# Kernel tuning notes

Hardware: AMD Instinct MI355X
Metric: run time of the kernel (lower is better)

The kernel has to match this reference:

```python
import jax, jax.numpy as jnp
import numpy as np

# ---- static config (matches init_kwargs) ----
N, E = 8192, 262144
IN_CH, MP_CH, HID, K = 128, 512, 256, 10
EPS, DELTA = 1e-3, 0.311
TV_COEFF, BAL_COEFF = 0.785, 0.514


def setup_inputs() -> dict:
    key = jax.random.key(0)
    ks = jax.random.split(key, 16)

    def p(k, shape):
        fan_in = shape[0] if len(shape) > 1 else shape[0]
        return (jax.random.normal(k, shape, jnp.float32) / np.sqrt(fan_in)).astype(jnp.float32)

    return {
        "x": jax.random.normal(ks[0], (N, IN_CH), jnp.float32),
        "edge_index": jax.random.randint(ks[1], (2, E), 0, N, jnp.int32),
        "edge_weight": jax.random.uniform(ks[2], (E,), jnp.float32),
        # GTVConv layer 1 / 2 (Linear weight + bias)
        "W1": p(ks[3], (IN_CH, MP_CH)), "b1": jnp.zeros((MP_CH,), jnp.float32),
        "W2": p(ks[4], (MP_CH, MP_CH)), "b2": jnp.zeros((MP_CH,), jnp.float32),
        # pooling MLP [512 -> 256 -> K], relu, no norm
        "Wm1": p(ks[5], (MP_CH, HID)), "bm1": jnp.zeros((HID,), jnp.float32),
        "Wm2": p(ks[6], (HID, K)), "bm2": jnp.zeros((K,), jnp.float32),
    }


def _gtv_conv(x, src, dst, w, W, b):
    """GTVConv: out = elu( h - delta*(D_G h - Gamma h) + b ),
    gamma_ij = w_ij / max(||h_i - h_j||_1, eps), h = x @ W."""
    h = x @ W                                   # [N, C]
    diff = jnp.sum(jnp.abs(h[src] - h[dst]), axis=-1)   # [E]
    gamma = w / jnp.maximum(diff, EPS)                  # [E]
    deg = jnp.zeros(h.shape[0], h.dtype).at[dst].add(gamma)          # [N]
    agg = jnp.zeros_like(h).at[dst].add(gamma[:, None] * h[src])     # Gamma @ h
    out = h - DELTA * (deg[:, None] * h - agg) + b
    return jax.nn.elu(out)


def reference(x, edge_index, edge_weight, W1, b1, W2, b2, Wm1, bm1, Wm2, bm2):
    src, dst = edge_index[0], edge_index[1]

    h = _gtv_conv(x, src, dst, edge_weight, W1, b1)
    h = _gtv_conv(h, src, dst, edge_weight, W2, b2)

    # pooling MLP -> cluster logits s
    s_logits = jax.nn.relu(h @ Wm1 + bm1) @ Wm2 + bm2   # [N, K]

    # dense adjacency (to_dense_adj: duplicate edges accumulate)
    adj = jnp.zeros((N, N), x.dtype).at[src, dst].add(edge_weight)

    s = jax.nn.softmax(s_logits, axis=-1)

    # total-variation loss: sum_ij a_ij * sum_k |s_ik - s_jk| / (2 * nnz(adj))
    tv = jnp.zeros((), x.dtype)
    for k in range(K):  # small fixed loop over clusters, avoids [N,N,K] tensor
        col = s[:, k]
        tv = tv + jnp.sum(adj * jnp.abs(col[:, None] - col[None, :]))
    n_edges = jax.lax.stop_gradient(jnp.count_nonzero(adj).astype(x.dtype))
    tv = tv / (2.0 * n_edges)

    # asymmetric-norm balance loss (AsymCheegerCut)
    idx = N // K + 1                         # rho-quantile index (static)
    quant = jnp.sort(s, axis=0)[N - idx]     # idx-th largest per cluster, [K]
    t = s - quant[None, :]
    asym = jnp.where(t >= 0, (K - 1) * t, -t)
    denom = float(N * (K - 1))
    bal = (denom - jnp.sum(asym)) / denom

    return s_logits, TV_COEFF * tv, BAL_COEFF * bal
```

## Files before the change

kernel.cpp:

```cpp
#include <hip/hip_runtime.h>

#define N_NODES 8192
#define N_EDGES 262144
#define IN_CH 128
#define MP_CH 512
#define HID 256
#define KCL 10
#define EPS_C 0.001f
#define DELTA_C 0.311f
#define TV_COEFF_C 0.785f
#define BAL_COEFF_C 0.514f
#define RANK1 7373

typedef __bf16 bf16x8 __attribute__((ext_vector_type(8)));
typedef float f32x4 __attribute__((ext_vector_type(4)));
typedef unsigned short ushort8 __attribute__((ext_vector_type(8)));

__device__ __forceinline__ float bf2f(unsigned short h) {
  union { unsigned int u; float f; } c; c.u = ((unsigned int)h) << 16; return c.f;
}
__device__ __forceinline__ unsigned short f2bf(float f) {
  union { float f; unsigned int u; } c; c.f = f;
  unsigned int r = c.u + 0x7fffu + ((c.u >> 16) & 1u);
  return (unsigned short)(r >> 16);
}

__global__ void prep_kernel(const float* __restrict__ x, const float* __restrict__ W1,
                            const float* __restrict__ W2, const float* __restrict__ Wm1,
                            unsigned short* __restrict__ xb, unsigned short* __restrict__ W1bt,
                            unsigned short* __restrict__ W2bt, unsigned short* __restrict__ Wm1bt,
                            const int* __restrict__ dst, int* __restrict__ cnt) {
  int i = blockIdx.x * 256 + threadIdx.x;
  if (i < 1048576) { xb[i] = f2bf(x[i]); return; }
  i -= 1048576;
  if (i < 65536) { int n = i >> 7, k = i & 127; W1bt[i] = f2bf(W1[k * MP_CH + n]); return; }
  i -= 65536;
  if (i < 262144) { int n = i >> 9, k = i & 511; W2bt[i] = f2bf(W2[k * MP_CH + n]); return; }
  i -= 262144;
  if (i < 131072) { int n = i >> 9, k = i & 511; Wm1bt[i] = f2bf(Wm1[k * HID + n]); return; }
  i -= 131072;
  if (i < N_EDGES) atomicAdd(&cnt[dst[i]], 1);
}

__global__ __launch_bounds__(1024) void scan_kernel(const int* __restrict__ cnt,
                                                    int* __restrict__ offs,
                                                    int* __restrict__ cursor) {
  __shared__ int ts[1024];
  int t = threadIdx.x;
  int v[8]; int s = 0;
#pragma unroll
  for (int j = 0; j < 8; ++j) { v[j] = cnt[t * 8 + j]; s += v[j]; }
  ts[t] = s; __syncthreads();
  for (int off = 1; off < 1024; off <<= 1) {
    int add = (t >= off) ? ts[t - off] : 0;
    __syncthreads();
    ts[t] += add;
    __syncthreads();
  }
  int base = ts[t] - s;
#pragma unroll
  for (int j = 0; j < 8; ++j) { offs[t * 8 + j] = base; cursor[t * 8 + j] = base; base += v[j]; }
  if (t == 1023) offs[N_NODES] = ts[1023];
}

__global__ void fill_kernel(const int* __restrict__ src, const int* __restrict__ dst,
                            const float* __restrict__ ew, int* __restrict__ cursor,
                            int2* __restrict__ esw) {
  for (int e = blockIdx.x * blockDim.x + threadIdx.x; e < N_EDGES; e += gridDim.x * blockDim.x) {
    int p = atomicAdd(&cursor[dst[e]], 1);
    esw[p] = make_int2(src[e], __float_as_int(ew[e]));
  }
}

__global__ __launch_bounds__(256) void gemm_bt(
    const unsigned short* __restrict__ A, const unsigned short* __restrict__ BT,
    float* __restrict__ C, unsigned short* __restrict__ Cb,
    const float* __restrict__ bias, int N, int K, int epi) {
  __shared__ unsigned short lsm[2 * 128 * 32];
  unsigned short* lA = lsm;
  unsigned short* lB = lsm + 128 * 32;
  int lane = threadIdx.x & 63;
  int wv = threadIdx.x >> 6;
  int tm = blockIdx.y * 128, tn = blockIdx.x * 128;
  int wm = (wv >> 1) * 64, wn = (wv & 1) * 64;
  int rA = lane & 15, quad = lane >> 4;
  f32x4 acc[4][4];
#pragma unroll
  for (int i = 0; i < 4; ++i)
#pragma unroll
    for (int j = 0; j < 4; ++j) acc[i][j] = (f32x4){0.f, 0.f, 0.f, 0.f};

  int arow = wv * 32 + (lane >> 2);
  int acol = (lane & 3) * 8;

  for (int k0 = 0; k0 < K; k0 += 32) {
#pragma unroll
    for (int c = 0; c < 2; ++c) {
      const unsigned short* ga = A + (size_t)(tm + arow + c * 16) * K + k0 + acol;
      __builtin_amdgcn_global_load_lds(
          (const __attribute__((address_space(1))) unsigned int*)ga,
          (__attribute__((address_space(3))) unsigned int*)(lA + (wv * 32 + c * 16) * 32),
          16, 0, 0);
      const unsigned short* gb = BT + (size_t)(tn + arow + c * 16) * K + k0 + acol;
      __builtin_amdgcn_global_load_lds(
          (const __attribute__((address_space(1))) unsigned int*)gb,
          (__attribute__((address_space(3))) unsigned int*)(lB + (wv * 32 + c * 16) * 32),
          16, 0, 0);
    }
    __syncthreads();
    bf16x8 af[4], bfr[4];
#pragma unroll
    for (int i = 0; i < 4; ++i)
      af[i] = *(const bf16x8*)(lA + (wm + i * 16 + rA) * 32 + quad * 8);
#pragma unroll
    for (int j = 0; j < 4; ++j)
      bfr[j] = *(const bf16x8*)(lB + (wn + j * 16 + rA) * 32 + quad * 8);
#pragma unroll
    for (int i = 0; i < 4; ++i)
#pragma unroll
      for (int j = 0; j < 4; ++j)
        acc[i][j] = __builtin_amdgcn_mfma_f32_16x16x32_bf16(af[i], bfr[j], acc[i][j], 0, 0, 0);
    __syncthreads();
  }

  if (epi == 1) {
#pragma unroll
    for (int i = 0; i < 4; ++i)
#pragma unroll
      for (int j = 0; j < 4; ++j)
#pragma unroll
        for (int r = 0; r < 4; ++r) {
          int row = tm + wm + i * 16 + quad * 4 + r;
          int col = tn + wn + j * 16 + rA;
          float v = acc[i][j][r] + bias[col];
          C[(size_t)row * N + col] = fmaxf(v, 0.f);
        }
  } else {
    float* fbuf = (float*)lsm;
    int band = threadIdx.x >> 7;
    int rrow = (threadIdx.x >> 3) & 15;
    int cg = threadIdx.x & 7;
#pragma unroll
    for (int i = 0; i < 4; ++i) {
#pragma unroll
      for (int j = 0; j < 4; ++j)
#pragma unroll
        for (int r = 0; r < 4; ++r)
          fbuf[(wv >> 1) * (16 * 128) + (quad * 4 + r) * 128 + (wn + j * 16 + rA)] =
              acc[i][j][r];
      __syncthreads();
      const float* sr = fbuf + band * (16 * 128) + rrow * 128 + cg * 16;
      unsigned short ov[16];
#pragma unroll
      for (int c = 0; c < 16; ++c) ov[c] = f2bf(sr[c]);
      size_t base = (size_t)(tm + band * 64 + i * 16 + rrow) * N + tn + cg * 16;
      *(ushort8*)(Cb + base) = *(ushort8*)ov;
      *(ushort8*)(Cb + base + 8) = *(ushort8*)(ov + 8);
      __syncthreads();
    }
  }
}

__global__ __launch_bounds__(256, 8) void gtv_node(
    const unsigned short* __restrict__ hb, const float* __restrict__ bias,
    const int2* __restrict__ esw, const int* __restrict__ offs,
    unsigned short* __restrict__ outb) {
  int lane = threadIdx.x & 63;
  int wv = threadIdx.x >> 6;
  int d = __builtin_amdgcn_readfirstlane(blockIdx.x * 4 + wv);
  ushort8 hdv = ((const ushort8*)(hb + (size_t)d * MP_CH))[lane];
  float hd[8], acc[8];
#pragma unroll
  for (int j = 0; j < 8; ++j) { hd[j] = bf2f(hdv[j]); acc[j] = 0.f; }
  int e0 = offs[d], e1 = offs[d + 1];
  int i = e0;
  for (; i + 1 < e1; i += 2) {
    int2 ma = esw[i], mb = esw[i + 1];
    float wa = __int_as_float(ma.y), wb = __int_as_float(mb.y);
    ushort8 va = ((const ushort8*)(hb + (size_t)ma.x * MP_CH))[lane];
    ushort8 vb = ((const ushort8*)(hb + (size_t)mb.x * MP_CH))[lane];
    float pa = 0.f, pb = 0.f;
#pragma unroll
    for (int j = 0; j < 8; ++j) {
      pa += fabsf(hd[j] - bf2f(va[j]));
      pb += fabsf(hd[j] - bf2f(vb[j]));
    }
#pragma unroll
    for (int m = 1; m < 64; m <<= 1) { pa += __shfl_xor(pa, m, 64); pb += __shfl_xor(pb, m, 64); }
    float ga = wa * __builtin_amdgcn_rcpf(fmaxf(pa, EPS_C));
    float gb = wb * __builtin_amdgcn_rcpf(fmaxf(pb, EPS_C));
#pragma unroll
    for (int j = 0; j < 8; ++j)
      acc[j] += ga * (hd[j] - bf2f(va[j])) + gb * (hd[j] - bf2f(vb[j]));
  }
  if (i < e1) {
    int2 m0 = esw[i];
    float w = __int_as_float(m0.y);
    ushort8 sv = ((const ushort8*)(hb + (size_t)m0.x * MP_CH))[lane];
    float part = 0.f;
#pragma unroll
    for (int j = 0; j < 8; ++j) part += fabsf(hd[j] - bf2f(sv[j]));
#pragma unroll
    for (int m = 1; m < 64; m <<= 1) part += __shfl_xor(part, m, 64);
    float g = w * __builtin_amdgcn_rcpf(fmaxf(part, EPS_C));
#pragma unroll
    for (int j = 0; j < 8; ++j) acc[j] += g * (hd[j] - bf2f(sv[j]));
  }
  const f32x4* br = (const f32x4*)(bias + lane * 8);
  f32x4 b0 = br[0], b1 = br[1];
  unsigned short ov[8];
#pragma unroll
  for (int j = 0; j < 8; ++j) {
    float bv = (j < 4) ? b0[j] : b1[j - 4];
    float o = hd[j] - DELTA_C * acc[j] + bv;
    o = (o > 0.f) ? o : (expf(o) - 1.f);
    ov[j] = f2bf(o);
  }
  *((ushort8*)(outb + (size_t)d * MP_CH) + lane) = *(ushort8*)ov;
}

__global__ __launch_bounds__(256) void gemm_small(
    const float* __restrict__ hm, const float* __restrict__ W,
    const float* __restrict__ b, float* __restrict__ out, float* __restrict__ s) {
  __shared__ float lw[HID * KCL];
  __shared__ float lb[KCL];
  for (int i = threadIdx.x; i < HID * KCL; i += 256) lw[i] = W[i];
  if (threadIdx.x < KCL) lb[threadIdx.x] = b[threadIdx.x];
  __syncthreads();
  int lane = threadIdx.x & 63, wv = threadIdx.x >> 6;
  int row = blockIdx.x * 4 + wv;
  f32x4 hv = *(const f32x4*)(hm + (size_t)row * HID + lane * 4);
  float p[KCL];
#pragma unroll
  for (int n = 0; n < KCL; ++n) {
    int k0 = lane * 4;
    p[n] = hv[0] * lw[(k0 + 0) * KCL + n] + hv[1] * lw[(k0 + 1) * KCL + n] +
           hv[2] * lw[(k0 + 2) * KCL + n] + hv[3] * lw[(k0 + 3) * KCL + n];
  }
#pragma unroll
  for (int n = 0; n < KCL; ++n)
#pragma unroll
    for (int m = 1; m < 64; m <<= 1) p[n] += __shfl_xor(p[n], m, 64);
  if (lane == 0) {
    float vv[KCL]; float mx = -1e30f;
#pragma unroll
    for (int n = 0; n < KCL; ++n) {
      vv[n] = p[n] + lb[n];
      out[(size_t)row * KCL + n] = vv[n];
      mx = fmaxf(mx, vv[n]);
    }
    float sum = 0.f;
#pragma unroll
    for (int n = 0; n < KCL; ++n) { vv[n] = expf(vv[n] - mx); sum += vv[n]; }
    float inv = 1.f / sum;
#pragma unroll
    for (int n = 0; n < KCL; ++n) s[(size_t)row * KCL + n] = vv[n] * inv;
  }
}

__global__ __launch_bounds__(1024) void tvquant_kernel(
    const int* __restrict__ src, const int* __restrict__ dst,
    const float* __restrict__ ew, const float* __restrict__ s,
    unsigned int* __restrict__ bitmap, float* __restrict__ scal) {
  __shared__ float fsh[16];
  __shared__ int wcnt[2][16];
  int t = threadIdx.x;
  int lane = t & 63, wv = t >> 6;
  if (blockIdx.x < 246) {
    float local = 0.f;
    for (int e = blockIdx.x * 1024 + t; e < N_EDGES; e += 246 * 1024) {
      int a = src[e], b = dst[e];
      float w = ew[e];
      const float* sa = s + (size_t)a * KCL;
      const float* sb = s + (size_t)b * KCL;
      float tv = 0.f;
#pragma unroll
      for (int k = 0; k < KCL; ++k) tv += fabsf(sa[k] - sb[k]);
      local += w * tv;
      if (w != 0.f) {
        unsigned int key = ((unsigned int)a << 13) | (unsigned int)b;
        atomicOr(&bitmap[key >> 5], 1u << (key & 31u));
      }
    }
#pragma unroll
    for (int m = 1; m < 64; m <<= 1) local += __shfl_xor(local, m, 64);
    if (lane == 0) fsh[wv] = local;
    __syncthreads();
    if (t == 0) {
      float tot = 0.f;
#pragma unroll
      for (int i2 = 0; i2 < 16; ++i2) tot += fsh[i2];
      atomicAdd(&scal[0], tot);
    }
  } else {
    int k = blockIdx.x - 246;
    unsigned int v[8];
#pragma unroll
    for (int j = 0; j < 8; ++j)
      v[j] = __float_as_uint(s[(size_t)(t + j * 1024) * KCL + k]);
    unsigned int lo = 0u, hi = 0x3F800000u;
    int p = 0;
    while (lo < hi) {
      unsigned int mid = (lo + hi) >> 1;
      int c = 0;
#pragma unroll
      for (int j = 0; j < 8; ++j) c += (v[j] <= mid) ? 1 : 0;
#pragma unroll
      for (int m = 1; m < 64; m <<= 1) c += __shfl_xor(c, m, 64);
      if (lane == 0) wcnt[p][wv] = c;
      __syncthreads();
      int tot = 0;
#pragma unroll
      for (int i2 = 0; i2 < 16; ++i2) tot += wcnt[p][i2];
      if (tot >= RANK1) hi = mid; else lo = mid + 1;
      p ^= 1;
    }
    float q = __uint_as_float(lo);
    float local = 0.f;
#pragma unroll
    for (int j = 0; j < 8; ++j) {
      float tt = __uint_as_float(v[j]) - q;
      local += (tt >= 0.f) ? 9.f * tt : -tt;
    }
#pragma unroll
    for (int m = 1; m < 64; m <<= 1) local += __shfl_xor(local, m, 64);
    if (lane == 0) fsh[wv] = local;
    __syncthreads();
    if (t == 0) {
      float tot = 0.f;
#pragma unroll
      for (int i2 = 0; i2 < 16; ++i2) tot += fsh[i2];
      atomicAdd(&scal[1], tot);
    }
  }
}

__global__ __launch_bounds__(1024) void popcfin_kernel(const unsigned int* __restrict__ bm,
                                                       float* __restrict__ scal,
                                                       float* __restrict__ out) {
  __shared__ int ish[16];
  int t = threadIdx.x;
  int lane = t & 63, wv = t >> 6;
  int local = 0;
  for (int i = blockIdx.x * 1024 + t; i < (1 << 21); i += 256 * 1024)
    local += __popc(bm[i]);
#pragma unroll
  for (int m = 1; m < 64; m <<= 1) local += __shfl_xor(local, m, 64);
  if (lane == 0) ish[wv] = local;
  __syncthreads();
  if (t == 0) {
    int tot = 0;
#pragma unroll
    for (int i2 = 0; i2 < 16; ++i2) tot += ish[i2];
    atomicAdd((int*)(scal + 2), tot);
    __threadfence();
    int d = atomicAdd((int*)(scal + 3), 1);
    if (d == 255) {
      float tv = scal[0], asym = scal[1];
      float nedges = (float)(*(int*)(scal + 2));
      out[N_NODES * KCL] = TV_COEFF_C * (tv / (2.f * nedges));
      out[N_NODES * KCL + 1] = BAL_COEFF_C * ((73728.f - asym) / 73728.f);
    }
  }
}

#define OFF_BM     ((size_t)0)
#define OFF_CNT    ((size_t)8388608)
#define OFF_SCAL   ((size_t)8421376)
#define OFF_OFFS   ((size_t)8421888)
#define OFF_CURSOR ((size_t)8454912)
#define OFF_HB     ((size_t)16777216)
#define OFF_OUTB   ((size_t)25165824)
#define OFF_HM     ((size_t)33554432)
#define OFF_XB     ((size_t)41943040)
#define OFF_W1BT   ((size_t)44040192)
#define OFF_W2BT   ((size_t)44171264)
#define OFF_WM1BT  ((size_t)44695552)
#define OFF_S      ((size_t)44957696)

extern "C" void kernel_launch(void* const* d_in, const int* in_sizes, int n_in,
                              void* d_out, int out_size, void* d_ws, size_t ws_size,
                              hipStream_t stream) {
  const float* x   = (const float*)d_in[0];
  const int*   ei  = (const int*)d_in[1];
  const float* ew  = (const float*)d_in[2];
  const float* W1  = (const float*)d_in[3];
  const float* b1  = (const float*)d_in[4];
  const float* W2  = (const float*)d_in[5];
  const float* b2  = (const float*)d_in[6];
  const float* Wm1 = (const float*)d_in[7];
  const float* bm1 = (const float*)d_in[8];
  const float* Wm2 = (const float*)d_in[9];
  const float* bm2 = (const float*)d_in[10];
  float* out = (float*)d_out;

  char* ws = (char*)d_ws;
  unsigned int*   bitmap = (unsigned int*)(ws + OFF_BM);
  int*            cnt    = (int*)(ws + OFF_CNT);
  float*          scal   = (float*)(ws + OFF_SCAL);
  int*            offs   = (int*)(ws + OFF_OFFS);
  int*            cursor = (int*)(ws + OFF_CURSOR);
  unsigned short* hb     = (unsigned short*)(ws + OFF_HB);
  unsigned short* outb   = (unsigned short*)(ws + OFF_OUTB);
  float*          hm     = (float*)(ws + OFF_HM);
  int2*           esw    = (int2*)(ws + OFF_HM);
  unsigned short* xb     = (unsigned short*)(ws + OFF_XB);
  unsigned short* W1bt   = (unsigned short*)(ws + OFF_W1BT);
  unsigned short* W2bt   = (unsigned short*)(ws + OFF_W2BT);
  unsigned short* Wm1bt  = (unsigned short*)(ws + OFF_WM1BT);
  float*          s      = (float*)(ws + OFF_S);

  const int* srcA = ei;
  const int* dstA = ei + N_EDGES;

  hipMemsetAsync(ws, 0, 8421632, stream);

  prep_kernel<<<6912, 256, 0, stream>>>(x, W1, W2, Wm1, xb, W1bt, W2bt, Wm1bt, dstA, cnt);
  scan_kernel<<<1, 1024, 0, stream>>>(cnt, offs, cursor);
  fill_kernel<<<1024, 256, 0, stream>>>(srcA, dstA, ew, cursor, esw);

  gemm_bt<<<dim3(MP_CH / 128, N_NODES / 128), 256, 0, stream>>>(
      xb, W1bt, nullptr, hb, nullptr, MP_CH, IN_CH, 2);
  gtv_node<<<N_NODES / 4, 256, 0, stream>>>(hb, b1, esw, offs, outb);
  gemm_bt<<<dim3(MP_CH / 128, N_NODES / 128), 256, 0, stream>>>(
      outb, W2bt, nullptr, hb, nullptr, MP_CH, MP_CH, 2);
  gtv_node<<<N_NODES / 4, 256, 0, stream>>>(hb, b2, esw, offs, outb);
  gemm_bt<<<dim3(HID / 128, N_NODES / 128), 256, 0, stream>>>(
      outb, Wm1bt, hm, nullptr, bm1, HID, MP_CH, 1);
  gemm_small<<<N_NODES / 4, 256, 0, stream>>>(hm, Wm2, bm2, out, s);

  tvquant_kernel<<<256, 1024, 0, stream>>>(srcA, dstA, ew, s, bitmap, scal);
  popcfin_kernel<<<256, 1024, 0, stream>>>(bitmap, scal, out);
}
```

Before: 261.5 us.

## Split each node's edges across two waves and schedule nodes by descending degree

The scan kernel now also counting-sorts nodes by in-degree (descending, capped bins) into a node order array. gtv_node assigns two waves per destination node, each processing half of its edge list, and combines partial accumulators through shared memory before the epilogue. Sorting by degree is meant to balance work across blocks, and splitting edges is meant to shorten per-node serial latency. The cost is a block-wide barrier, extra LDS traffic, twice as many waves, and a serial prefix loop in the single-block scan.

```diff
diff --git a/kernel.cpp b/kernel.cpp
--- a/kernel.cpp
+++ b/kernel.cpp
@@ -11,6 +11,7 @@
 #define TV_COEFF_C 0.785f
 #define BAL_COEFF_C 0.514f
 #define RANK1 7373
+#define DBINS 80
 
 typedef __bf16 bf16x8 __attribute__((ext_vector_type(8)));
 typedef float f32x4 __attribute__((ext_vector_type(4)));
@@ -44,12 +45,15 @@
 
 __global__ __launch_bounds__(1024) void scan_kernel(const int* __restrict__ cnt,
                                                     int* __restrict__ offs,
-                                                    int* __restrict__ cursor) {
+                                                    int* __restrict__ cursor,
+                                                    int* __restrict__ nodeorder) {
   __shared__ int ts[1024];
+  __shared__ int dh[DBINS];
   int t = threadIdx.x;
   int v[8]; int s = 0;
 #pragma unroll
   for (int j = 0; j < 8; ++j) { v[j] = cnt[t * 8 + j]; s += v[j]; }
+  if (t < DBINS) dh[t] = 0;
   ts[t] = s; __syncthreads();
   for (int off = 1; off < 1024; off <<= 1) {
     int add = (t >= off) ? ts[t - off] : 0;
@@ -59,8 +63,24 @@
   }
   int base = ts[t] - s;
 #pragma unroll
-  for (int j = 0; j < 8; ++j) { offs[t * 8 + j] = base; cursor[t * 8 + j] = base; base += v[j]; }
+  for (int j = 0; j < 8; ++j) {
+    offs[t * 8 + j] = base; cursor[t * 8 + j] = base; base += v[j];
+    int key = v[j] < (DBINS - 1) ? v[j] : (DBINS - 1);
+    atomicAdd(&dh[(DBINS - 1) - key], 1);
+  }
   if (t == 1023) offs[N_NODES] = ts[1023];
+  __syncthreads();
+  if (t == 0) {
+    int acc0 = 0;
+    for (int b = 0; b < DBINS; ++b) { int c = dh[b]; dh[b] = acc0; acc0 += c; }
+  }
+  __syncthreads();
+#pragma unroll
+  for (int j = 0; j < 8; ++j) {
+    int key = v[j] < (DBINS - 1) ? v[j] : (DBINS - 1);
+    int pos = atomicAdd(&dh[(DBINS - 1) - key], 1);
+    nodeorder[pos] = t * 8 + j;
+  }
 }
 
 __global__ void fill_kernel(const int* __restrict__ src, const int* __restrict__ dst,
@@ -164,15 +184,21 @@
 __global__ __launch_bounds__(256, 8) void gtv_node(
     const unsigned short* __restrict__ hb, const float* __restrict__ bias,
     const int2* __restrict__ esw, const int* __restrict__ offs,
-    unsigned short* __restrict__ outb) {
+    const int* __restrict__ nodeorder, unsigned short* __restrict__ outb) {
+  __shared__ float sacc[2][MP_CH];
   int lane = threadIdx.x & 63;
   int wv = threadIdx.x >> 6;
-  int d = __builtin_amdgcn_readfirstlane(blockIdx.x * 4 + wv);
+  int pair = wv >> 1;
+  int half = wv & 1;
+  int d = __builtin_amdgcn_readfirstlane(nodeorder[blockIdx.x * 2 + pair]);
   ushort8 hdv = ((const ushort8*)(hb + (size_t)d * MP_CH))[lane];
   float hd[8], acc[8];
 #pragma unroll
   for (int j = 0; j < 8; ++j) { hd[j] = bf2f(hdv[j]); acc[j] = 0.f; }
-  int e0 = offs[d], e1 = offs[d + 1];
+  int n0 = offs[d], n1 = offs[d + 1];
+  int mid = n0 + ((n1 - n0 + 1) >> 1);
+  int e0 = half ? mid : n0;
+  int e1 = half ? n1 : mid;
   int i = e0;
   for (; i + 1 < e1; i += 2) {
     int2 ma = esw[i], mb = esw[i + 1];
@@ -206,17 +232,25 @@
 #pragma unroll
     for (int j = 0; j < 8; ++j) acc[j] += g * (hd[j] - bf2f(sv[j]));
   }
-  const f32x4* br = (const f32x4*)(bias + lane * 8);
-  f32x4 b0 = br[0], b1 = br[1];
-  unsigned short ov[8];
-#pragma unroll
-  for (int j = 0; j < 8; ++j) {
-    float bv = (j < 4) ? b0[j] : b1[j - 4];
-    float o = hd[j] - DELTA_C * acc[j] + bv;
-    o = (o > 0.f) ? o : (expf(o) - 1.f);
-    ov[j] = f2bf(o);
-  }
-  *((ushort8*)(outb + (size_t)d * MP_CH) + lane) = *(ushort8*)ov;
+  if (half) {
+#pragma unroll
+    for (int j = 0; j < 8; ++j) sacc[pair][lane * 8 + j] = acc[j];
+  }
+  __syncthreads();
+  if (!half) {
+    const f32x4* br = (const f32x4*)(bias + lane * 8);
+    f32x4 b0 = br[0], b1 = br[1];
+    unsigned short ov[8];
+#pragma unroll
+    for (int j = 0; j < 8; ++j) {
+      float tot = acc[j] + sacc[pair][lane * 8 + j];
+      float bv = (j < 4) ? b0[j] : b1[j - 4];
+      float o = hd[j] - DELTA_C * tot + bv;
+      o = (o > 0.f) ? o : (expf(o) - 1.f);
+      ov[j] = f2bf(o);
+    }
+    *((ushort8*)(outb + (size_t)d * MP_CH) + lane) = *(ushort8*)ov;
+  }
 }
 
 __global__ __launch_bounds__(256) void gemm_small(
@@ -369,6 +403,7 @@
 #define OFF_SCAL   ((size_t)8421376)
 #define OFF_OFFS   ((size_t)8421888)
 #define OFF_CURSOR ((size_t)8454912)
+#define OFF_NORD   ((size_t)8487936)
 #define OFF_HB     ((size_t)16777216)
 #define OFF_OUTB   ((size_t)25165824)
 #define OFF_HM     ((size_t)33554432)
@@ -400,6 +435,7 @@
   float*          scal   = (float*)(ws + OFF_SCAL);
   int*            offs   = (int*)(ws + OFF_OFFS);
   int*            cursor = (int*)(ws + OFF_CURSOR);
+  int*            nord   = (int*)(ws + OFF_NORD);
   unsigned short* hb     = (unsigned short*)(ws + OFF_HB);
   unsigned short* outb   = (unsigned short*)(ws + OFF_OUTB);
   float*          hm     = (float*)(ws + OFF_HM);
@@ -416,15 +452,15 @@
   hipMemsetAsync(ws, 0, 8421632, stream);
 
   prep_kernel<<<6912, 256, 0, stream>>>(x, W1, W2, Wm1, xb, W1bt, W2bt, Wm1bt, dstA, cnt);
-  scan_kernel<<<1, 1024, 0, stream>>>(cnt, offs, cursor);
+  scan_kernel<<<1, 1024, 0, stream>>>(cnt, offs, cursor, nord);
   fill_kernel<<<1024, 256, 0, stream>>>(srcA, dstA, ew, cursor, esw);
 
   gemm_bt<<<dim3(MP_CH / 128, N_NODES / 128), 256, 0, stream>>>(
       xb, W1bt, nullptr, hb, nullptr, MP_CH, IN_CH, 2);
-  gtv_node<<<N_NODES / 4, 256, 0, stream>>>(hb, b1, esw, offs, outb);
+  gtv_node<<<N_NODES / 2, 256, 0, stream>>>(hb, b1, esw, offs, nord, outb);
   gemm_bt<<<dim3(MP_CH / 128, N_NODES / 128), 256, 0, stream>>>(
       outb, W2bt, nullptr, hb, nullptr, MP_CH, MP_CH, 2);
-  gtv_node<<<N_NODES / 4, 256, 0, stream>>>(hb, b2, esw, offs, outb);
+  gtv_node<<<N_NODES / 2, 256, 0, stream>>>(hb, b2, esw, offs, nord, outb);
   gemm_bt<<<dim3(HID / 128, N_NODES / 128), 256, 0, stream>>>(
       outb, Wm1bt, hm, nullptr, bm1, HID, MP_CH, 1);
   gemm_small<<<N_NODES / 4, 256, 0, stream>>>(hm, Wm2, bm2, out, s);
```

New measurement: 259.4 us, median of 2. No clear change (-0.8%).
